# Kernel tuning notes

Measured on AMD Instinct MI355X. Metric: run time of the kernel, lower is better.

## Reference

```python
import jax, jax.numpy as jnp
import numpy as np

C = 256          # channels
K = 7            # involution kernel size
DIL = 1          # dilation
PAD = (K // 2) * DIL
RED = 4          # reduction ratio for kernel generation
GC = 16          # group channels
G = C // GC      # involution groups
EPS = 1e-5


def setup_inputs() -> dict:
    key = jax.random.key(0)
    ks = jax.random.split(key, 6)
    B, L = 8, 8192
    Cr = C // RED
    x = jax.random.normal(ks[0], (B, C, L), dtype=jnp.float32)
    w_reduce = jax.random.normal(ks[1], (Cr, C), dtype=jnp.float32) * 0.05
    w_span = jax.random.normal(ks[2], (G * K, Cr), dtype=jnp.float32) * 0.05
    prelu_a = jnp.asarray(0.25, dtype=jnp.float32)
    ln_gamma = jnp.ones((C,), dtype=jnp.float32)
    ln_beta = jnp.zeros((C,), dtype=jnp.float32)
    w_main = jax.random.normal(ks[3], (C, C), dtype=jnp.float32) * 0.05
    w_skip = jax.random.normal(ks[4], (C, C), dtype=jnp.float32) * 0.05
    return {"x": x, "w_reduce": w_reduce, "w_span": w_span,
            "prelu_a": prelu_a, "ln_gamma": ln_gamma, "ln_beta": ln_beta,
            "w_main": w_main, "w_skip": w_skip}


def reference(x, w_reduce, w_span, prelu_a, ln_gamma, ln_beta, w_main, w_skip):
    B, Cc, L = x.shape
    # --- Involution1D: dynamic per-position kernel generation (1x1 reduce + ReLU + 1x1 span) ---
    h = jax.nn.relu(jnp.einsum('rc,bcl->brl', w_reduce, x))              # (B, C/RED, L)
    ker = jnp.einsum('kr,brl->bkl', w_span, h).reshape(B, G, K, L)       # (B, G, K, L)
    # --- unfold x into sliding windows (stride 1, same padding) ---
    xp = jnp.pad(x, ((0, 0), (0, 0), (PAD, PAD)))
    xu = jnp.stack([jax.lax.dynamic_slice_in_dim(xp, k * DIL, L, axis=2)
                    for k in range(K)], axis=2)                           # (B, C, K, L)
    xu = xu.reshape(B, G, GC, K, L)
    out = jnp.einsum('bgkl,bgckl->bgcl', ker, xu).reshape(B, Cc, L)      # weighted sum over K
    # --- PReLU (single shared slope) ---
    out = jnp.where(out >= 0, out, prelu_a * out)
    # --- LayerNorm over channel dim (transpose->LN(C)->transpose) ---
    mu = jnp.mean(out, axis=1, keepdims=True)
    var = jnp.var(out, axis=1, keepdims=True)
    outn = (out - mu) * jax.lax.rsqrt(var + EPS)
    outn = outn * ln_gamma[None, :, None] + ln_beta[None, :, None]
    # --- pointwise convs + residual ---
    main_out = jnp.einsum('oc,bcl->bol', w_main, outn) + x
    skip = jnp.einsum('oc,bcl->bol', w_skip, outn)
    return main_out, skip
```

## Files before the change

### kernel.cpp

```cpp
#include <hip/hip_runtime.h>
#include <stdint.h>

#define C_DIM 256
#define L_DIM 8192
#define B_DIM 8
#define SKIP_OFF ((size_t)B_DIM * C_DIM * L_DIM)

using short8  = __attribute__((ext_vector_type(8))) short;
using floatx4 = __attribute__((ext_vector_type(4))) float;
typedef unsigned short ushort_t;

__device__ __forceinline__ ushort_t f2bf(float f) {
    union { float f; uint32_t u; } v; v.f = f;
    uint32_t u = v.u;
    return (ushort_t)((u + 0x7fff + ((u >> 16) & 1)) >> 16);
}
__device__ __forceinline__ float bf2f(ushort_t h) {
    union { uint32_t u; float f; } v; v.u = ((uint32_t)h) << 16;
    return v.f;
}

__device__ __forceinline__ int fragaddr(int l, int c) {
    return ((((l >> 4) * 8 + (c >> 5)) * 16 + (l & 15)) * 4 + ((c >> 3) & 3)) * 8 + (c & 7);
}

__global__ __launch_bounds__(256) void k0_prep(const float* __restrict__ wm,
                                               const float* __restrict__ wk,
                                               const float* __restrict__ wr,
                                               const float* __restrict__ wsp,
                                               ushort_t* __restrict__ wb,
                                               ushort_t* __restrict__ wrb,
                                               ushort_t* __restrict__ wsb) {
    int i = blockIdx.x * 256 + threadIdx.x;
    if (i < 65536) wb[i] = f2bf(wm[i]);
    else if (i < 131072) wb[i] = f2bf(wk[i - 65536]);
    else if (i < 147456) wrb[i - 131072] = f2bf(wr[i - 131072]);
    else if (i < 155648) {
        int j = i - 147456;
        int r = j >> 6, cc = j & 63;
        wsb[j] = (r < 112) ? f2bf(wsp[r * 64 + cc]) : (ushort_t)0;
    }
}

#define KS_STR 40
__global__ __launch_bounds__(256) void k_fused(const float* __restrict__ x,
                                               const ushort_t* __restrict__ wrb,
                                               const ushort_t* __restrict__ wsb,
                                               const ushort_t* __restrict__ wb,
                                               const float* __restrict__ pa,
                                               const float* __restrict__ gamma,
                                               const float* __restrict__ beta,
                                               float* __restrict__ out) {
    __shared__ __align__(16) ushort_t xsF[8192];
    __shared__ __align__(16) ushort_t hTF[2048];
    __shared__ __align__(16) ushort_t ks[112 * KS_STR];

    int t = threadIdx.x;
    int b = blockIdx.x >> 8;
    int l0 = (blockIdx.x & 255) * 32;
    const float* xb = x + (size_t)b * C_DIM * L_DIM;

    int c = t;
    float haloL[3], haloR[3];
#pragma unroll
    for (int j = 0; j < 3; ++j) {
        int ll = l0 - 3 + j;
        haloL[j] = (ll >= 0) ? xb[(size_t)c * L_DIM + ll] : 0.f;
        int rr = l0 + 32 + j;
        haloR[j] = (rr < L_DIM) ? xb[(size_t)c * L_DIM + rr] : 0.f;
    }

    {
        int lo = (t & 7) * 4;
        int cb = t >> 3;
#pragma unroll
        for (int j = 0; j < 8; ++j) {
            int cc = cb + j * 32;
            float4 v = *(const float4*)&xb[(size_t)cc * L_DIM + l0 + lo];
            xsF[fragaddr(lo + 0, cc)] = f2bf(v.x);
            xsF[fragaddr(lo + 1, cc)] = f2bf(v.y);
            xsF[fragaddr(lo + 2, cc)] = f2bf(v.z);
            xsF[fragaddr(lo + 3, cc)] = f2bf(v.w);
        }
    }
    __syncthreads();

    int w = t >> 6, lane = t & 63, lr = lane & 15, quad = lane >> 4;

    {
        short8 af[8];
#pragma unroll
        for (int s = 0; s < 8; ++s)
            af[s] = *(const short8*)&wrb[(w * 16 + lr) * 256 + s * 32 + quad * 8];
#pragma unroll
        for (int nt = 0; nt < 2; ++nt) {
            floatx4 a4 = {0.f, 0.f, 0.f, 0.f};
#pragma unroll
            for (int s = 0; s < 8; ++s) {
                short8 bf = *(const short8*)&xsF[(((nt * 8 + s) * 16 + lr) * 4 + quad) * 8];
                a4 = __builtin_amdgcn_mfma_f32_16x16x32_bf16(af[s], bf, a4, 0, 0, 0);
            }
            int r0 = w * 16 + quad * 4;
            int sK = r0 >> 5, qK = (r0 >> 3) & 3, j0 = r0 & 7;
            ushort4 hv;
            hv.x = f2bf(fmaxf(a4[0], 0.f));
            hv.y = f2bf(fmaxf(a4[1], 0.f));
            hv.z = f2bf(fmaxf(a4[2], 0.f));
            hv.w = f2bf(fmaxf(a4[3], 0.f));
            *(ushort4*)&hTF[(((nt * 2 + sK) * 16 + lr) * 4 + qK) * 8 + j0] = hv;
        }
    }
    __syncthreads();

#pragma unroll
    for (int mi = 0; mi < 2; ++mi) {
        int mt = w * 2 + mi;
        if (mt == 7) break;
        short8 aw[2];
#pragma unroll
        for (int s = 0; s < 2; ++s)
            aw[s] = *(const short8*)&wsb[(mt * 16 + lr) * 64 + s * 32 + quad * 8];
#pragma unroll
        for (int nt = 0; nt < 2; ++nt) {
            floatx4 a4 = {0.f, 0.f, 0.f, 0.f};
#pragma unroll
            for (int s = 0; s < 2; ++s) {
                short8 bf = *(const short8*)&hTF[(((nt * 2 + s) * 16 + lr) * 4 + quad) * 8];
                a4 = __builtin_amdgcn_mfma_f32_16x16x32_bf16(aw[s], bf, a4, 0, 0, 0);
            }
            int r0 = mt * 16 + quad * 4;
            int n  = nt * 16 + lr;
#pragma unroll
            for (int r = 0; r < 4; ++r)
                ks[(r0 + r) * KS_STR + n] = f2bf(a4[r]);
        }
    }
    __syncthreads();

    int g = c >> 4;
    float aslope = pa[0], gam = gamma[c], bet = beta[c];
    float xwin[38];
    xwin[0] = haloL[0]; xwin[1] = haloL[1]; xwin[2] = haloL[2];
#pragma unroll
    for (int j = 0; j < 32; ++j) xwin[3 + j] = bf2f(xsF[fragaddr(j, c)]);
    xwin[35] = haloR[0]; xwin[36] = haloR[1]; xwin[37] = haloR[2];

    float acc[32];
#pragma unroll
    for (int j = 0; j < 32; ++j) acc[j] = 0.f;
#pragma unroll
    for (int k = 0; k < 7; ++k) {
        const ushort_t* krow = &ks[(g * 7 + k) * KS_STR];
#pragma unroll
        for (int ch = 0; ch < 4; ++ch) {
            ushort4 kp0 = *(const ushort4*)&krow[ch * 8];
            ushort4 kp1 = *(const ushort4*)&krow[ch * 8 + 4];
            float kv0 = bf2f(kp0.x), kv1 = bf2f(kp0.y), kv2 = bf2f(kp0.z), kv3 = bf2f(kp0.w);
            float kv4 = bf2f(kp1.x), kv5 = bf2f(kp1.y), kv6 = bf2f(kp1.z), kv7 = bf2f(kp1.w);
            acc[ch*8+0] = fmaf(kv0, xwin[ch*8 + 0 + k], acc[ch*8+0]);
            acc[ch*8+1] = fmaf(kv1, xwin[ch*8 + 1 + k], acc[ch*8+1]);
            acc[ch*8+2] = fmaf(kv2, xwin[ch*8 + 2 + k], acc[ch*8+2]);
            acc[ch*8+3] = fmaf(kv3, xwin[ch*8 + 3 + k], acc[ch*8+3]);
            acc[ch*8+4] = fmaf(kv4, xwin[ch*8 + 4 + k], acc[ch*8+4]);
            acc[ch*8+5] = fmaf(kv5, xwin[ch*8 + 5 + k], acc[ch*8+5]);
            acc[ch*8+6] = fmaf(kv6, xwin[ch*8 + 6 + k], acc[ch*8+6]);
            acc[ch*8+7] = fmaf(kv7, xwin[ch*8 + 7 + k], acc[ch*8+7]);
        }
    }
    __syncthreads();

#pragma unroll
    for (int j = 0; j < 32; ++j) {
        acc[j] = acc[j] >= 0.f ? acc[j] : aslope * acc[j];
        xsF[fragaddr(j, c)] = f2bf(acc[j]);
    }
    __syncthreads();

    float* red1   = (float*)hTF;
    float* red2   = red1 + 256;
    float* mean_s = red2 + 256;
    float* rstd_s = mean_s + 32;
    {
        int lloc = t >> 3, seg = t & 7;
        float s1 = 0.f, s2 = 0.f;
#pragma unroll
        for (int q = 0; q < 4; ++q) {
            ushort4 v0 = *(const ushort4*)&xsF[fragaddr(lloc, seg * 32 + q * 8)];
            ushort4 v1 = *(const ushort4*)&xsF[fragaddr(lloc, seg * 32 + q * 8 + 4)];
            float f0 = bf2f(v0.x), f1 = bf2f(v0.y), f2v = bf2f(v0.z), f3 = bf2f(v0.w);
            float f4 = bf2f(v1.x), f5 = bf2f(v1.y), f6 = bf2f(v1.z), f7 = bf2f(v1.w);
            s1 += ((f0 + f1) + (f2v + f3)) + ((f4 + f5) + (f6 + f7));
            s2 += f0*f0 + f1*f1 + f2v*f2v + f3*f3 + f4*f4 + f5*f5 + f6*f6 + f7*f7;
        }
        red1[t] = s1; red2[t] = s2;
    }
    __syncthreads();
    if (t < 32) {
        float s1 = 0.f, s2 = 0.f;
#pragma unroll
        for (int i = 0; i < 8; ++i) { s1 += red1[t * 8 + i]; s2 += red2[t * 8 + i]; }
        float mu  = s1 * (1.f / 256.f);
        float var = s2 * (1.f / 256.f) - mu * mu;
        mean_s[t] = mu;
        rstd_s[t] = rsqrtf(var + 1e-5f);
    }
    __syncthreads();
#pragma unroll
    for (int j = 0; j < 32; ++j) {
        float v = (acc[j] - mean_s[j]) * rstd_s[j] * gam + bet;
        xsF[fragaddr(j, c)] = f2bf(v);
    }
    __syncthreads();

#pragma unroll
    for (int mi = 0; mi < 8; ++mi) {
        int mt = w * 8 + mi;
        const ushort_t* arow = wb + (size_t)(mt * 16 + lr) * 256 + quad * 8;
        short8 a[8];
#pragma unroll
        for (int s = 0; s < 8; ++s) a[s] = *(const short8*)(arow + s * 32);
#pragma unroll
        for (int nt = 0; nt < 2; ++nt) {
            floatx4 a4 = {0.f, 0.f, 0.f, 0.f};
#pragma unroll
            for (int s = 0; s < 8; ++s) {
                short8 bfr = *(const short8*)&xsF[(((nt * 8 + s) * 16 + lr) * 4 + quad) * 8];
                a4 = __builtin_amdgcn_mfma_f32_16x16x32_bf16(a[s], bfr, a4, 0, 0, 0);
            }
            int m = mt * 16 + quad * 4;
            int l = l0 + nt * 16 + lr;
            if (mt < 16) {
                size_t base = ((size_t)b * C_DIM + m) * L_DIM + l;
#pragma unroll
                for (int r = 0; r < 4; ++r)
                    out[base + (size_t)r * L_DIM] = a4[r] + x[base + (size_t)r * L_DIM];
            } else {
                size_t base = SKIP_OFF + ((size_t)b * C_DIM + (m - 256)) * L_DIM + l;
#pragma unroll
                for (int r = 0; r < 4; ++r)
                    out[base + (size_t)r * L_DIM] = a4[r];
            }
        }
    }
}

extern "C" void kernel_launch(void* const* d_in, const int* in_sizes, int n_in,
                              void* d_out, int out_size, void* d_ws, size_t ws_size,
                              hipStream_t stream) {
    const float* x     = (const float*)d_in[0];
    const float* w_red = (const float*)d_in[1];
    const float* w_spn = (const float*)d_in[2];
    const float* pa    = (const float*)d_in[3];
    const float* gam   = (const float*)d_in[4];
    const float* bet   = (const float*)d_in[5];
    const float* w_m   = (const float*)d_in[6];
    const float* w_s   = (const float*)d_in[7];
    float* out = (float*)d_out;

    char* ws = (char*)d_ws;
    ushort_t* wb  = (ushort_t*)(ws);
    ushort_t* wrb = (ushort_t*)(ws + 262144);
    ushort_t* wsb = (ushort_t*)(ws + 294912);

    k0_prep<<<608, 256, 0, stream>>>(w_m, w_s, w_red, w_spn, wb, wrb, wsb);
    k_fused<<<2048, 256, 0, stream>>>(x, wrb, wsb, wb, pa, gam, bet, out);
}
```

Measured before the change: 279.1 us.

## Split fused kernel into front stage and register-tiled bf16 MFMA GEMM

The fused kernel is split in two. The front stage writes the normalized bf16 activations to a workspace buffer in fragment layout. A separate GEMM kernel then loads 64 positions per block and computes a 4x4 MFMA tile per wave, with weights pre-swizzled into fragment order so they load contiguously. This targets the poor weight reuse of the old epilogue, which reloaded 256-wide weight rows per 32-position tile, at the cost of an extra global round trip for the activations (about 32 MB written and read) and an extra launch.

```diff
diff --git a/kernel.cpp b/kernel.cpp
--- a/kernel.cpp
+++ b/kernel.cpp
@@ -28,14 +28,18 @@
                                                const float* __restrict__ wk,
                                                const float* __restrict__ wr,
                                                const float* __restrict__ wsp,
-                                               ushort_t* __restrict__ wb,
+                                               ushort_t* __restrict__ wbF,
                                                ushort_t* __restrict__ wrb,
                                                ushort_t* __restrict__ wsb) {
     int i = blockIdx.x * 256 + threadIdx.x;
-    if (i < 65536) wb[i] = f2bf(wm[i]);
-    else if (i < 131072) wb[i] = f2bf(wk[i - 65536]);
-    else if (i < 147456) wrb[i - 131072] = f2bf(wr[i - 131072]);
-    else if (i < 155648) {
+    if (i < 131072) {
+        int m = i >> 8, k = i & 255;
+        float v = (m < 256) ? wm[m * 256 + k] : wk[(m - 256) * 256 + k];
+        int mt = m >> 4, lr = m & 15, s = k >> 5, q = (k >> 3) & 3, j = k & 7;
+        wbF[(((mt * 8 + s) * 16 + lr) * 32) + q * 8 + j] = f2bf(v);
+    } else if (i < 147456) {
+        wrb[i - 131072] = f2bf(wr[i - 131072]);
+    } else if (i < 155648) {
         int j = i - 147456;
         int r = j >> 6, cc = j & 63;
         wsb[j] = (r < 112) ? f2bf(wsp[r * 64 + cc]) : (ushort_t)0;
@@ -43,14 +47,13 @@
 }
 
 #define KS_STR 40
-__global__ __launch_bounds__(256) void k_fused(const float* __restrict__ x,
+__global__ __launch_bounds__(256) void k_front(const float* __restrict__ x,
                                                const ushort_t* __restrict__ wrb,
                                                const ushort_t* __restrict__ wsb,
-                                               const ushort_t* __restrict__ wb,
                                                const float* __restrict__ pa,
                                                const float* __restrict__ gamma,
                                                const float* __restrict__ beta,
-                                               float* __restrict__ out) {
+                                               ushort_t* __restrict__ xnG) {
     __shared__ __align__(16) ushort_t xsF[8192];
     __shared__ __align__(16) ushort_t hTF[2048];
     __shared__ __align__(16) ushort_t ks[112 * KS_STR];
@@ -212,33 +215,88 @@
     }
     __syncthreads();
 
-#pragma unroll
-    for (int mi = 0; mi < 8; ++mi) {
-        int mt = w * 8 + mi;
-        const ushort_t* arow = wb + (size_t)(mt * 16 + lr) * 256 + quad * 8;
-        short8 a[8];
-#pragma unroll
-        for (int s = 0; s < 8; ++s) a[s] = *(const short8*)(arow + s * 32);
-#pragma unroll
-        for (int nt = 0; nt < 2; ++nt) {
-            floatx4 a4 = {0.f, 0.f, 0.f, 0.f};
-#pragma unroll
-            for (int s = 0; s < 8; ++s) {
-                short8 bfr = *(const short8*)&xsF[(((nt * 8 + s) * 16 + lr) * 4 + quad) * 8];
-                a4 = __builtin_amdgcn_mfma_f32_16x16x32_bf16(a[s], bfr, a4, 0, 0, 0);
+    {
+        const uint4* src = (const uint4*)xsF;
+        uint4* dst = (uint4*)(xnG + (size_t)blockIdx.x * 8192);
+#pragma unroll
+        for (int j = 0; j < 4; ++j) dst[t + j * 256] = src[t + j * 256];
+    }
+}
+
+__global__ __launch_bounds__(256) void k_gemm(const ushort_t* __restrict__ xnG,
+                                              const ushort_t* __restrict__ wbF,
+                                              const float* __restrict__ x,
+                                              float* __restrict__ out) {
+    __shared__ __align__(16) ushort_t xnLds[16384];
+
+    int t = threadIdx.x;
+    int b  = blockIdx.x >> 7;
+    int lt = blockIdx.x & 127;
+    int l0 = lt * 64;
+
+    {
+        const uint4* src = (const uint4*)(xnG + (size_t)(b * 256 + lt * 2) * 8192);
+        uint4* dst = (uint4*)xnLds;
+#pragma unroll
+        for (int j = 0; j < 8; ++j) dst[t + j * 256] = src[t + j * 256];
+    }
+    __syncthreads();
+
+    int w = t >> 6, lane = t & 63, lr = lane & 15, quad = lane >> 4;
+
+#pragma unroll
+    for (int grp = 0; grp < 2; ++grp) {
+        int mtbase = w * 8 + grp * 4;
+        floatx4 acc[4][4];
+#pragma unroll
+        for (int mi = 0; mi < 4; ++mi)
+#pragma unroll
+            for (int nt = 0; nt < 4; ++nt)
+                acc[mi][nt] = (floatx4){0.f, 0.f, 0.f, 0.f};
+
+#pragma unroll
+        for (int s = 0; s < 8; ++s) {
+            short8 Bf[4];
+#pragma unroll
+            for (int nt = 0; nt < 4; ++nt)
+                Bf[nt] = *(const short8*)&xnLds[(nt >> 1) * 8192 +
+                         ((((nt & 1) * 8 + s) * 16 + lr) * 4 + quad) * 8];
+            short8 Af[4];
+#pragma unroll
+            for (int mi = 0; mi < 4; ++mi)
+                Af[mi] = *(const short8*)&wbF[(size_t)(((mtbase + mi) * 8 + s) * 16 + lr) * 32 + quad * 8];
+#pragma unroll
+            for (int mi = 0; mi < 4; ++mi)
+#pragma unroll
+                for (int nt = 0; nt < 4; ++nt)
+                    acc[mi][nt] = __builtin_amdgcn_mfma_f32_16x16x32_bf16(Af[mi], Bf[nt], acc[mi][nt], 0, 0, 0);
+        }
+
+        if (mtbase < 16) {
+#pragma unroll
+            for (int mi = 0; mi < 4; ++mi) {
+                int m = (mtbase + mi) * 16 + quad * 4;
+#pragma unroll
+                for (int nt = 0; nt < 4; ++nt) {
+                    int l = l0 + nt * 16 + lr;
+                    size_t base = ((size_t)b * C_DIM + m) * L_DIM + l;
+#pragma unroll
+                    for (int r = 0; r < 4; ++r)
+                        out[base + (size_t)r * L_DIM] = acc[mi][nt][r] + x[base + (size_t)r * L_DIM];
+                }
             }
-            int m = mt * 16 + quad * 4;
-            int l = l0 + nt * 16 + lr;
-            if (mt < 16) {
-                size_t base = ((size_t)b * C_DIM + m) * L_DIM + l;
-#pragma unroll
-                for (int r = 0; r < 4; ++r)
-                    out[base + (size_t)r * L_DIM] = a4[r] + x[base + (size_t)r * L_DIM];
-            } else {
-                size_t base = SKIP_OFF + ((size_t)b * C_DIM + (m - 256)) * L_DIM + l;
-#pragma unroll
-                for (int r = 0; r < 4; ++r)
-                    out[base + (size_t)r * L_DIM] = a4[r];
+        } else {
+#pragma unroll
+            for (int mi = 0; mi < 4; ++mi) {
+                int m = (mtbase + mi) * 16 + quad * 4 - 256;
+#pragma unroll
+                for (int nt = 0; nt < 4; ++nt) {
+                    int l = l0 + nt * 16 + lr;
+                    size_t base = SKIP_OFF + ((size_t)b * C_DIM + m) * L_DIM + l;
+#pragma unroll
+                    for (int r = 0; r < 4; ++r)
+                        out[base + (size_t)r * L_DIM] = acc[mi][nt][r];
+                }
             }
         }
     }
@@ -258,10 +316,12 @@
     float* out = (float*)d_out;
 
     char* ws = (char*)d_ws;
-    ushort_t* wb  = (ushort_t*)(ws);
+    ushort_t* wbF = (ushort_t*)(ws);
     ushort_t* wrb = (ushort_t*)(ws + 262144);
     ushort_t* wsb = (ushort_t*)(ws + 294912);
-
-    k0_prep<<<608, 256, 0, stream>>>(w_m, w_s, w_red, w_spn, wb, wrb, wsb);
-    k_fused<<<2048, 256, 0, stream>>>(x, wrb, wsb, wb, pa, gam, bet, out);
-}
+    ushort_t* xnG = (ushort_t*)(ws + 311296);
+
+    k0_prep<<<608, 256, 0, stream>>>(w_m, w_s, w_red, w_spn, wbF, wrb, wsb);
+    k_front<<<2048, 256, 0, stream>>>(x, wrb, wsb, pa, gam, bet, xnG);
+    k_gemm<<<1024, 256, 0, stream>>>(xnG, wbF, x, out);
+}
```

Result: faster. 262.9 us (-5.8%).
